# Performance work log

Measured on AMD Instinct MI355X. Metric: run time of the kernel, lower is better.

The kernel has to match this reference:

```python
import jax, jax.numpy as jnp
import numpy as np

LATDIM = 128
ANCHOR_SET_NUM = 64
N_NODES = 10000

def setup_inputs() -> dict:
    key = jax.random.key(0)
    k1, k2, k3, k4, k5 = jax.random.split(key, 5)
    embeds = jax.random.normal(k1, (N_NODES, LATDIM), dtype=jnp.float32)
    dists_array = jax.random.uniform(k2, (ANCHOR_SET_NUM, N_NODES), dtype=jnp.float32)
    W_hidden = jax.random.normal(k3, (LATDIM, 2 * LATDIM), dtype=jnp.float32) * 0.05
    b_hidden = jax.random.normal(k4, (LATDIM,), dtype=jnp.float32) * 0.05
    anchorset_id = jax.random.randint(k5, (ANCHOR_SET_NUM,), 0, N_NODES, dtype=jnp.int64 if jax.config.jax_enable_x64 else jnp.int32)
    return {"embeds": embeds, "dists_array": dists_array, "W_hidden": W_hidden,
            "b_hidden": b_hidden, "anchorset_id": anchorset_id}

def reference(embeds, dists_array, W_hidden, b_hidden, anchorset_id):
    A, N = dists_array.shape
    d = embeds.shape[1]
    set_ids_emb = embeds[anchorset_id]                       # [A, d] anchor gather
    # messages[i, j] = set_ids_emb[j] * dists[j, i]
    messages = set_ids_emb[None, :, :] * dists_array.T[:, :, None]   # [N, A, d]
    # faithful to torch: embeds.repeat(A,1).reshape(-1, A, d) -> embeds[(i*A+j) % N]
    self_feature = jnp.tile(embeds, (A, 1)).reshape(N, A, d)          # [N, A, d]
    m = jnp.concatenate([messages, self_feature], axis=-1)            # [N, A, 2d]
    h = jnp.einsum('nak,ok->nao', m, W_hidden) + b_hidden             # [N, A, d]
    return jnp.mean(h, axis=1)                                        # [N, d]
```

## Files before the change

kernel.cpp:

```cpp
#include <hip/hip_runtime.h>

#define LATDIM 128
#define ANUM   64
#define NNODES 10000
#define PERIOD 625
#define TN     16
#define ABLK   64
#define SBLK   625


__global__ __launch_bounds__(256) void prep_kernel(
    const float* __restrict__ embeds,
    const float* __restrict__ W,
    const float* __restrict__ b,
    const int*   __restrict__ anchor,
    float* __restrict__ P,
    float* __restrict__ T2b)
{
    __shared__ float X_s[LATDIM];
    __shared__ float R_s[LATDIM];
    __shared__ float Xp[8][LATDIM];
    const int tid = threadIdx.x;
    const float4* X_s4 = (const float4*)X_s;

    if (blockIdx.x < ABLK) {
        const int a = blockIdx.x;
        if (tid < 32) {
            ((float4*)X_s)[tid] =
                *((const float4*)(embeds + (size_t)anchor[a] * LATDIM) + tid);
        }
        __syncthreads();

        const int o = tid & 127;
        const int h = tid >> 7;
        const float4* Wr = (const float4*)(W + (size_t)o * (2 * LATDIM) + h * 64);
        float acc = 0.f;
        #pragma unroll
        for (int k4 = 0; k4 < 16; ++k4) {
            float4 w4 = Wr[k4];
            float4 x4 = X_s4[h * 16 + k4];
            acc += w4.x * x4.x + w4.y * x4.y + w4.z * x4.z + w4.w * x4.w;
        }
        if (h == 1) R_s[o] = acc;
        __syncthreads();
        if (h == 0) P[(size_t)a * LATDIM + o] = acc + R_s[o];
    } else {
        const int s = blockIdx.x - ABLK;
        const int row0 = (64 * s) % NNODES;

        const int c4 = tid & 31;
        const int hg = tid >> 5;
        float4 sum = {0.f, 0.f, 0.f, 0.f};
        #pragma unroll
        for (int i = 0; i < 8; ++i) {
            int row = row0 + 8 * i + hg;
            if (row >= NNODES) row -= NNODES;
            float4 v = *((const float4*)(embeds + (size_t)row * LATDIM) + c4);
            sum.x += v.x; sum.y += v.y; sum.z += v.z; sum.w += v.w;
        }
        ((float4*)&Xp[hg][0])[c4] = sum;
        __syncthreads();
        if (tid < LATDIM) {
            float t = Xp[0][tid];
            #pragma unroll
            for (int g = 1; g < 8; ++g) t += Xp[g][tid];
            X_s[tid] = t;
        }
        __syncthreads();

        const int o = tid & 127;
        const int h = tid >> 7;
        const float4* Wr =
            (const float4*)(W + (size_t)o * (2 * LATDIM) + LATDIM + h * 64);
        float acc = 0.f;
        #pragma unroll
        for (int k4 = 0; k4 < 16; ++k4) {
            float4 w4 = Wr[k4];
            float4 x4 = X_s4[h * 16 + k4];
            acc += w4.x * x4.x + w4.y * x4.y + w4.z * x4.z + w4.w * x4.w;
        }
        if (h == 1) R_s[o] = acc;
        __syncthreads();
        if (h == 0)
            T2b[(size_t)s * LATDIM + o] =
                b[o] + (acc + R_s[o]) * (1.0f / ANUM);
    }
}

__global__ __launch_bounds__(256) void main_kernel(
    const float* __restrict__ dists,
    const float* __restrict__ P,
    const float* __restrict__ T2b,
    float* __restrict__ out)
{
    __shared__ float P_s[ANUM * LATDIM];
    const int tid = threadIdx.x;

    {
        float4* P_s4 = (float4*)P_s;
        const float4* Pg = (const float4*)P;
        #pragma unroll
        for (int it = 0; it < (ANUM * LATDIM / 4) / 256; ++it)
            P_s4[it * 256 + tid] = Pg[it * 256 + tid];
    }
    __syncthreads();

    const int lane = tid & 63;
    const int w    = __builtin_amdgcn_readfirstlane(tid >> 6);
    const int o    = (w & 1) * 64 + lane;
    const int nc   = w >> 1;
    const int nb   = blockIdx.x * TN + nc * 8;

    float acc[8] = {};
    #pragma unroll 4
    for (int a = 0; a < ANUM; ++a) {
        const float p = P_s[a * LATDIM + o];
        const float* __restrict__ drow = dists + (size_t)a * NNODES + nb;
        #pragma unroll
        for (int j = 0; j < 8; ++j)
            acc[j] += drow[j] * p;
    }

    #pragma unroll
    for (int j = 0; j < 8; ++j) {
        const int n = nb + j;
        const int s = n % PERIOD;
        out[(size_t)n * LATDIM + o] =
            acc[j] * (1.0f / ANUM) + T2b[(size_t)s * LATDIM + o];
    }
}

extern "C" void kernel_launch(void* const* d_in, const int* in_sizes, int n_in,
                              void* d_out, int out_size, void* d_ws, size_t ws_size,
                              hipStream_t stream) {
    const float* embeds = (const float*)d_in[0];
    const float* dists  = (const float*)d_in[1];
    const float* W      = (const float*)d_in[2];
    const float* b      = (const float*)d_in[3];
    const int*   anchor = (const int*)d_in[4];
    float* out = (float*)d_out;

    float* P   = (float*)d_ws;
    float* T2b = P + ANUM * LATDIM;

    prep_kernel<<<ABLK + SBLK, 256, 0, stream>>>(embeds, W, b, anchor, P, T2b);
    main_kernel<<<NNODES / TN, 256, 0, stream>>>(dists, P, T2b, out);
}
```

Before: 82.37 us.

## Fuse prep and main kernels with a grid-wide atomic barrier

Merges the precompute kernel and the main accumulation kernel into a single launch of 625 blocks. Each block computes one T2b row (plus a P row for the first 64 blocks), then all blocks wait at a software grid barrier built from an atomic counter before reading P. The dists tile is also staged in shared memory with vectorized loads, and the anchor loop is fully unrolled. This removes one kernel launch and the gap between kernels, but adds a memset, relies on all 625 blocks being co-resident, and adds spin-wait time at the barrier.

```diff
diff --git a/kernel.cpp b/kernel.cpp
--- a/kernel.cpp
+++ b/kernel.cpp
@@ -5,49 +5,34 @@
 #define NNODES 10000
 #define PERIOD 625
 #define TN     16
-#define ABLK   64
 #define SBLK   625
 
 
-__global__ __launch_bounds__(256) void prep_kernel(
+__global__ __launch_bounds__(256) void fused_kernel(
     const float* __restrict__ embeds,
+    const float* __restrict__ dists,
     const float* __restrict__ W,
     const float* __restrict__ b,
     const int*   __restrict__ anchor,
     float* __restrict__ P,
-    float* __restrict__ T2b)
+    float* __restrict__ T2b,
+    unsigned int* __restrict__ cnt,
+    float* __restrict__ out)
 {
-    __shared__ float X_s[LATDIM];
-    __shared__ float R_s[LATDIM];
-    __shared__ float Xp[8][LATDIM];
+    __shared__ float P_s[ANUM * LATDIM];
+    __shared__ float D_s[ANUM * TN];
+    float* X_s = P_s;
+    float* R_s = P_s + LATDIM;
+    float (*Xp)[LATDIM] = (float (*)[LATDIM])(P_s + 2 * LATDIM);
+
     const int tid = threadIdx.x;
+    const int bid = blockIdx.x;
+    const int o   = tid & 127;
+    const int h   = tid >> 7;
     const float4* X_s4 = (const float4*)X_s;
 
-    if (blockIdx.x < ABLK) {
-        const int a = blockIdx.x;
-        if (tid < 32) {
-            ((float4*)X_s)[tid] =
-                *((const float4*)(embeds + (size_t)anchor[a] * LATDIM) + tid);
-        }
-        __syncthreads();
-
-        const int o = tid & 127;
-        const int h = tid >> 7;
-        const float4* Wr = (const float4*)(W + (size_t)o * (2 * LATDIM) + h * 64);
-        float acc = 0.f;
-        #pragma unroll
-        for (int k4 = 0; k4 < 16; ++k4) {
-            float4 w4 = Wr[k4];
-            float4 x4 = X_s4[h * 16 + k4];
-            acc += w4.x * x4.x + w4.y * x4.y + w4.z * x4.z + w4.w * x4.w;
-        }
-        if (h == 1) R_s[o] = acc;
-        __syncthreads();
-        if (h == 0) P[(size_t)a * LATDIM + o] = acc + R_s[o];
-    } else {
-        const int s = blockIdx.x - ABLK;
-        const int row0 = (64 * s) % NNODES;
-
+    {
+        const int row0 = (64 * bid) % NNODES;
         const int c4 = tid & 31;
         const int hg = tid >> 5;
         float4 sum = {0.f, 0.f, 0.f, 0.f};
@@ -68,8 +53,6 @@
         }
         __syncthreads();
 
-        const int o = tid & 127;
-        const int h = tid >> 7;
         const float4* Wr =
             (const float4*)(W + (size_t)o * (2 * LATDIM) + LATDIM + h * 64);
         float acc = 0.f;
@@ -82,19 +65,45 @@
         if (h == 1) R_s[o] = acc;
         __syncthreads();
         if (h == 0)
-            T2b[(size_t)s * LATDIM + o] =
+            T2b[(size_t)bid * LATDIM + o] =
                 b[o] + (acc + R_s[o]) * (1.0f / ANUM);
     }
-}
 
-__global__ __launch_bounds__(256) void main_kernel(
-    const float* __restrict__ dists,
-    const float* __restrict__ P,
-    const float* __restrict__ T2b,
-    float* __restrict__ out)
-{
-    __shared__ float P_s[ANUM * LATDIM];
-    const int tid = threadIdx.x;
+    if (bid < ANUM) {
+        __syncthreads();
+        if (tid < 32) {
+            ((float4*)X_s)[tid] =
+                *((const float4*)(embeds + (size_t)anchor[bid] * LATDIM) + tid);
+        }
+        __syncthreads();
+        const float4* Wr = (const float4*)(W + (size_t)o * (2 * LATDIM) + h * 64);
+        float acc = 0.f;
+        #pragma unroll
+        for (int k4 = 0; k4 < 16; ++k4) {
+            float4 w4 = Wr[k4];
+            float4 x4 = X_s4[h * 16 + k4];
+            acc += w4.x * x4.x + w4.y * x4.y + w4.z * x4.z + w4.w * x4.w;
+        }
+        if (h == 1) R_s[o] = acc;
+        __syncthreads();
+        if (h == 0) P[(size_t)bid * LATDIM + o] = acc + R_s[o];
+    }
+
+    __syncthreads();
+    if (tid == 0) {
+        __threadfence();
+        __hip_atomic_fetch_add(cnt, 1u, __ATOMIC_ACQ_REL,
+                               __HIP_MEMORY_SCOPE_AGENT);
+        int guard = 0;
+        while (__hip_atomic_load(cnt, __ATOMIC_ACQUIRE,
+                                 __HIP_MEMORY_SCOPE_AGENT) < (unsigned)SBLK &&
+               guard < (1 << 24)) {
+            __builtin_amdgcn_s_sleep(4);
+            ++guard;
+        }
+    }
+    __syncthreads();
+    __threadfence();
 
     {
         float4* P_s4 = (float4*)P_s;
@@ -102,31 +111,35 @@
         #pragma unroll
         for (int it = 0; it < (ANUM * LATDIM / 4) / 256; ++it)
             P_s4[it * 256 + tid] = Pg[it * 256 + tid];
+        ((float4*)D_s)[tid] = *(const float4*)(
+            dists + (size_t)(tid >> 2) * NNODES + bid * TN + 4 * (tid & 3));
     }
     __syncthreads();
 
     const int lane = tid & 63;
     const int w    = __builtin_amdgcn_readfirstlane(tid >> 6);
-    const int o    = (w & 1) * 64 + lane;
+    const int oo   = (w & 1) * 64 + lane;
     const int nc   = w >> 1;
-    const int nb   = blockIdx.x * TN + nc * 8;
+    const int nb   = bid * TN + nc * 8;
 
     float acc[8] = {};
-    #pragma unroll 4
+    #pragma unroll
     for (int a = 0; a < ANUM; ++a) {
-        const float p = P_s[a * LATDIM + o];
-        const float* __restrict__ drow = dists + (size_t)a * NNODES + nb;
-        #pragma unroll
-        for (int j = 0; j < 8; ++j)
-            acc[j] += drow[j] * p;
+        const float p = P_s[a * LATDIM + oo];
+        const float4 d0 = ((const float4*)(D_s + a * TN + nc * 8))[0];
+        const float4 d1 = ((const float4*)(D_s + a * TN + nc * 8))[1];
+        acc[0] += d0.x * p; acc[1] += d0.y * p;
+        acc[2] += d0.z * p; acc[3] += d0.w * p;
+        acc[4] += d1.x * p; acc[5] += d1.y * p;
+        acc[6] += d1.z * p; acc[7] += d1.w * p;
     }
 
     #pragma unroll
     for (int j = 0; j < 8; ++j) {
         const int n = nb + j;
         const int s = n % PERIOD;
-        out[(size_t)n * LATDIM + o] =
-            acc[j] * (1.0f / ANUM) + T2b[(size_t)s * LATDIM + o];
+        out[(size_t)n * LATDIM + oo] =
+            acc[j] * (1.0f / ANUM) + T2b[(size_t)s * LATDIM + oo];
     }
 }
 
@@ -142,7 +155,9 @@
 
     float* P   = (float*)d_ws;
     float* T2b = P + ANUM * LATDIM;
+    unsigned int* cnt = (unsigned int*)(T2b + PERIOD * LATDIM);
 
-    prep_kernel<<<ABLK + SBLK, 256, 0, stream>>>(embeds, W, b, anchor, P, T2b);
-    main_kernel<<<NNODES / TN, 256, 0, stream>>>(dists, P, T2b, out);
+    hipMemsetAsync(cnt, 0, sizeof(unsigned int), stream);
+    fused_kernel<<<SBLK, 256, 0, stream>>>(embeds, dists, W, b, anchor,
+                                           P, T2b, cnt, out);
 }
```

Measured after the change: 210.2 us. 2.55x slower.

## Fuse prep and main kernels into one per-residue-class kernel

Applied to the files above, without the earlier changes.

Replaces the two-kernel pipeline with a single kernel launched over the 625 residue classes. Each block handles the 16 nodes sharing a self-feature residue. It computes the anchor-weighted dist sums G in shared memory, then applies W to both G and the shared self-feature sum, with a bias-and-mean epilogue. This removes a launch and the workspace round trip. In exchange, every block reloads all 64 anchor embeddings and the full W, the dists reads become strided, and blockIdx is remapped across XCDs.

```diff
diff --git a/kernel.cpp b/kernel.cpp
--- a/kernel.cpp
+++ b/kernel.cpp
@@ -4,52 +4,39 @@
 #define ANUM   64
 #define NNODES 10000
 #define PERIOD 625
-#define TN     16
-#define ABLK   64
-#define SBLK   625
+#define NJ     16
 
 
-__global__ __launch_bounds__(256) void prep_kernel(
+__global__ __launch_bounds__(256) void fused_kernel(
     const float* __restrict__ embeds,
+    const float* __restrict__ dists,
     const float* __restrict__ W,
     const float* __restrict__ b,
     const int*   __restrict__ anchor,
-    float* __restrict__ P,
-    float* __restrict__ T2b)
+    float* __restrict__ out)
 {
-    __shared__ float X_s[LATDIM];
-    __shared__ float R_s[LATDIM];
-    __shared__ float Xp[8][LATDIM];
+    __shared__ float EA[ANUM * LATDIM];
+    __shared__ float G_s[NJ * LATDIM];
+    __shared__ float D_s[ANUM * NJ];
+    __shared__ float S_s[LATDIM];
+    __shared__ int   An[ANUM];
+
     const int tid = threadIdx.x;
-    const float4* X_s4 = (const float4*)X_s;
+    const int orig = blockIdx.x;
+    const int xcd = orig & 7, ii = orig >> 3;
+    const int s = (xcd == 0) ? ii : (79 + (xcd - 1) * 78 + ii);
 
-    if (blockIdx.x < ABLK) {
-        const int a = blockIdx.x;
-        if (tid < 32) {
-            ((float4*)X_s)[tid] =
-                *((const float4*)(embeds + (size_t)anchor[a] * LATDIM) + tid);
-        }
-        __syncthreads();
-
-        const int o = tid & 127;
-        const int h = tid >> 7;
-        const float4* Wr = (const float4*)(W + (size_t)o * (2 * LATDIM) + h * 64);
-        float acc = 0.f;
-        #pragma unroll
-        for (int k4 = 0; k4 < 16; ++k4) {
-            float4 w4 = Wr[k4];
-            float4 x4 = X_s4[h * 16 + k4];
-            acc += w4.x * x4.x + w4.y * x4.y + w4.z * x4.z + w4.w * x4.w;
-        }
-        if (h == 1) R_s[o] = acc;
-        __syncthreads();
-        if (h == 0) P[(size_t)a * LATDIM + o] = acc + R_s[o];
-    } else {
-        const int s = blockIdx.x - ABLK;
+    if (tid < ANUM) An[tid] = anchor[tid];
+    #pragma unroll
+    for (int it = 0; it < 4; ++it) {
+        int idx = it * 256 + tid;
+        int a = idx >> 4, j = idx & 15;
+        D_s[a * NJ + j] = dists[(size_t)a * NNODES + (s + PERIOD * j)];
+    }
+    float (*Xp)[LATDIM] = (float (*)[LATDIM])G_s;
+    {
         const int row0 = (64 * s) % NNODES;
-
-        const int c4 = tid & 31;
-        const int hg = tid >> 5;
+        const int c4 = tid & 31, hg = tid >> 5;
         float4 sum = {0.f, 0.f, 0.f, 0.f};
         #pragma unroll
         for (int i = 0; i < 8; ++i) {
@@ -59,74 +46,81 @@
             sum.x += v.x; sum.y += v.y; sum.z += v.z; sum.w += v.w;
         }
         ((float4*)&Xp[hg][0])[c4] = sum;
-        __syncthreads();
-        if (tid < LATDIM) {
-            float t = Xp[0][tid];
-            #pragma unroll
-            for (int g = 1; g < 8; ++g) t += Xp[g][tid];
-            X_s[tid] = t;
-        }
-        __syncthreads();
-
-        const int o = tid & 127;
-        const int h = tid >> 7;
-        const float4* Wr =
-            (const float4*)(W + (size_t)o * (2 * LATDIM) + LATDIM + h * 64);
-        float acc = 0.f;
-        #pragma unroll
-        for (int k4 = 0; k4 < 16; ++k4) {
-            float4 w4 = Wr[k4];
-            float4 x4 = X_s4[h * 16 + k4];
-            acc += w4.x * x4.x + w4.y * x4.y + w4.z * x4.z + w4.w * x4.w;
-        }
-        if (h == 1) R_s[o] = acc;
-        __syncthreads();
-        if (h == 0)
-            T2b[(size_t)s * LATDIM + o] =
-                b[o] + (acc + R_s[o]) * (1.0f / ANUM);
-    }
-}
-
-__global__ __launch_bounds__(256) void main_kernel(
-    const float* __restrict__ dists,
-    const float* __restrict__ P,
-    const float* __restrict__ T2b,
-    float* __restrict__ out)
-{
-    __shared__ float P_s[ANUM * LATDIM];
-    const int tid = threadIdx.x;
-
-    {
-        float4* P_s4 = (float4*)P_s;
-        const float4* Pg = (const float4*)P;
-        #pragma unroll
-        for (int it = 0; it < (ANUM * LATDIM / 4) / 256; ++it)
-            P_s4[it * 256 + tid] = Pg[it * 256 + tid];
     }
     __syncthreads();
 
-    const int lane = tid & 63;
-    const int w    = __builtin_amdgcn_readfirstlane(tid >> 6);
-    const int o    = (w & 1) * 64 + lane;
-    const int nc   = w >> 1;
-    const int nb   = blockIdx.x * TN + nc * 8;
+    if (tid < LATDIM) {
+        float t = Xp[0][tid];
+        #pragma unroll
+        for (int g = 1; g < 8; ++g) t += Xp[g][tid];
+        S_s[tid] = t;
+    }
+    #pragma unroll
+    for (int it = 0; it < 8; ++it) {
+        int idx = it * 256 + tid;
+        int a = idx >> 5, c4 = idx & 31;
+        ((float4*)EA)[a * 32 + c4] =
+            *((const float4*)(embeds + (size_t)An[a] * LATDIM) + c4);
+    }
+    __syncthreads();
 
-    float acc[8] = {};
-    #pragma unroll 4
-    for (int a = 0; a < ANUM; ++a) {
-        const float p = P_s[a * LATDIM + o];
-        const float* __restrict__ drow = dists + (size_t)a * NNODES + nb;
+    {
+        const int k  = tid & 127;
+        const int jh = tid >> 7;
+        float g[8] = {};
         #pragma unroll
-        for (int j = 0; j < 8; ++j)
-            acc[j] += drow[j] * p;
+        for (int a = 0; a < ANUM; ++a) {
+            const float  ea = EA[a * LATDIM + k];
+            const float4 d0 = ((const float4*)(D_s + a * NJ + jh * 8))[0];
+            const float4 d1 = ((const float4*)(D_s + a * NJ + jh * 8))[1];
+            g[0] += d0.x * ea; g[1] += d0.y * ea;
+            g[2] += d0.z * ea; g[3] += d0.w * ea;
+            g[4] += d1.x * ea; g[5] += d1.y * ea;
+            g[6] += d1.z * ea; g[7] += d1.w * ea;
+        }
+        #pragma unroll
+        for (int jj = 0; jj < 8; ++jj)
+            G_s[(jh * 8 + jj) * LATDIM + k] = g[jj];
     }
+    __syncthreads();
 
-    #pragma unroll
-    for (int j = 0; j < 8; ++j) {
-        const int n = nb + j;
-        const int s = n % PERIOD;
-        out[(size_t)n * LATDIM + o] =
-            acc[j] * (1.0f / ANUM) + T2b[(size_t)s * LATDIM + o];
+    {
+        const int o = tid & 127;
+        const int h = tid >> 7;
+        const float4* Wr1 = (const float4*)(W + (size_t)o * (2 * LATDIM) + h * 64);
+        const float4* Wr2 = (const float4*)(W + (size_t)o * (2 * LATDIM) + LATDIM + h * 64);
+        const float4* S4  = (const float4*)S_s;
+        const float4* G4  = (const float4*)G_s;
+        float acc[NJ] = {};
+        float sacc = 0.f;
+        #pragma unroll
+        for (int q = 0; q < 16; ++q) {
+            const float4 w1 = Wr1[q];
+            const float4 w2 = Wr2[q];
+            const float4 sv = S4[h * 16 + q];
+            sacc += sv.x*w2.x + sv.y*w2.y + sv.z*w2.z + sv.w*w2.w;
+            #pragma unroll
+            for (int j = 0; j < NJ; ++j) {
+                const float4 gv = G4[j * 32 + h * 16 + q];
+                acc[j] += gv.x*w1.x + gv.y*w1.y + gv.z*w1.z + gv.w*w1.w;
+            }
+        }
+        float* R = EA;
+        if (h == 1) {
+            #pragma unroll
+            for (int j = 0; j < NJ; ++j)
+                R[j * LATDIM + o] = acc[j] + sacc;
+        }
+        __syncthreads();
+        if (h == 0) {
+            const float bias = b[o];
+            #pragma unroll
+            for (int j = 0; j < NJ; ++j) {
+                const int n = s + PERIOD * j;
+                out[(size_t)n * LATDIM + o] =
+                    bias + (acc[j] + sacc + R[j * LATDIM + o]) * (1.0f / ANUM);
+            }
+        }
     }
 }
 
@@ -140,9 +134,6 @@
     const int*   anchor = (const int*)d_in[4];
     float* out = (float*)d_out;
 
-    float* P   = (float*)d_ws;
-    float* T2b = P + ANUM * LATDIM;
-
-    prep_kernel<<<ABLK + SBLK, 256, 0, stream>>>(embeds, W, b, anchor, P, T2b);
-    main_kernel<<<NNODES / TN, 256, 0, stream>>>(dists, P, T2b, out);
+    (void)d_ws; (void)ws_size;
+    fused_kernel<<<PERIOD, 256, 0, stream>>>(embeds, dists, W, b, anchor, out);
 }
```

After: 88.13 us. 7.0% more time.

## Fuse periodic self-term computation into main kernel with period-strided node tiling

Applied to the files above, without the earlier changes.

The prep kernel is split: a small kernel computes only the per-anchor projections P. The self-feature projection T2b is now computed inside the main kernel. Each main block handles one period residue s and its 16 nodes n = s + 625*j, so the T2 term is computed once per block and kept in shared memory instead of round-tripping through global memory. Dists columns are staged into shared memory with strided gathers, and blocks are remapped so that XCD-adjacent blocks get contiguous residues. This trades uncoalesced dists loads and strided output rows for removing the T2b intermediate and a larger prep launch.

```diff
diff --git a/kernel.cpp b/kernel.cpp
--- a/kernel.cpp
+++ b/kernel.cpp
@@ -4,52 +4,72 @@
 #define ANUM   64
 #define NNODES 10000
 #define PERIOD 625
-#define TN     16
-#define ABLK   64
-#define SBLK   625
+#define NJ     16
 
 
-__global__ __launch_bounds__(256) void prep_kernel(
+__global__ __launch_bounds__(256) void p_kernel(
     const float* __restrict__ embeds,
     const float* __restrict__ W,
-    const float* __restrict__ b,
     const int*   __restrict__ anchor,
-    float* __restrict__ P,
-    float* __restrict__ T2b)
+    float* __restrict__ P)
 {
     __shared__ float X_s[LATDIM];
     __shared__ float R_s[LATDIM];
+    const int tid = threadIdx.x;
+    const int a = blockIdx.x;
+    if (tid < 32)
+        ((float4*)X_s)[tid] =
+            *((const float4*)(embeds + (size_t)anchor[a] * LATDIM) + tid);
+    __syncthreads();
+    const int o = tid & 127, h = tid >> 7;
+    const float4* Wr = (const float4*)(W + (size_t)o * (2 * LATDIM) + h * 64);
+    const float4* X4 = (const float4*)X_s;
+    float acc = 0.f;
+    #pragma unroll
+    for (int q = 0; q < 16; ++q) {
+        float4 w4 = Wr[q], x4 = X4[h * 16 + q];
+        acc += w4.x*x4.x + w4.y*x4.y + w4.z*x4.z + w4.w*x4.w;
+    }
+    if (h == 1) R_s[o] = acc;
+    __syncthreads();
+    if (h == 0) P[(size_t)a * LATDIM + o] = acc + R_s[o];
+}
+
+__global__ __launch_bounds__(256) void main_kernel(
+    const float* __restrict__ embeds,
+    const float* __restrict__ dists,
+    const float* __restrict__ W,
+    const float* __restrict__ b,
+    const float* __restrict__ P,
+    float* __restrict__ out)
+{
+    __shared__ float P_s[ANUM * LATDIM];
     __shared__ float Xp[8][LATDIM];
+    __shared__ float D_s[ANUM * NJ];
+    __shared__ float S_s[LATDIM];
+    __shared__ float T2_s[LATDIM];
+    __shared__ float Rb[LATDIM];
+
     const int tid = threadIdx.x;
-    const float4* X_s4 = (const float4*)X_s;
+    const int orig = blockIdx.x;
+    const int xcd = orig & 7, ii = orig >> 3;
+    const int s = (xcd == 0) ? ii : (79 + (xcd - 1) * 78 + ii);
 
-    if (blockIdx.x < ABLK) {
-        const int a = blockIdx.x;
-        if (tid < 32) {
-            ((float4*)X_s)[tid] =
-                *((const float4*)(embeds + (size_t)anchor[a] * LATDIM) + tid);
-        }
-        __syncthreads();
-
-        const int o = tid & 127;
-        const int h = tid >> 7;
-        const float4* Wr = (const float4*)(W + (size_t)o * (2 * LATDIM) + h * 64);
-        float acc = 0.f;
+    {
+        float4* P4 = (float4*)P_s; const float4* Pg = (const float4*)P;
         #pragma unroll
-        for (int k4 = 0; k4 < 16; ++k4) {
-            float4 w4 = Wr[k4];
-            float4 x4 = X_s4[h * 16 + k4];
-            acc += w4.x * x4.x + w4.y * x4.y + w4.z * x4.z + w4.w * x4.w;
-        }
-        if (h == 1) R_s[o] = acc;
-        __syncthreads();
-        if (h == 0) P[(size_t)a * LATDIM + o] = acc + R_s[o];
-    } else {
-        const int s = blockIdx.x - ABLK;
+        for (int it = 0; it < 8; ++it)
+            P4[it * 256 + tid] = Pg[it * 256 + tid];
+    }
+    #pragma unroll
+    for (int it = 0; it < 4; ++it) {
+        int idx = it * 256 + tid;
+        int a = idx >> 4, j = idx & 15;
+        D_s[a * NJ + j] = dists[(size_t)a * NNODES + (s + PERIOD * j)];
+    }
+    {
         const int row0 = (64 * s) % NNODES;
-
-        const int c4 = tid & 31;
-        const int hg = tid >> 5;
+        const int c4 = tid & 31, hg = tid >> 5;
         float4 sum = {0.f, 0.f, 0.f, 0.f};
         #pragma unroll
         for (int i = 0; i < 8; ++i) {
@@ -59,49 +79,31 @@
             sum.x += v.x; sum.y += v.y; sum.z += v.z; sum.w += v.w;
         }
         ((float4*)&Xp[hg][0])[c4] = sum;
-        __syncthreads();
-        if (tid < LATDIM) {
-            float t = Xp[0][tid];
-            #pragma unroll
-            for (int g = 1; g < 8; ++g) t += Xp[g][tid];
-            X_s[tid] = t;
-        }
-        __syncthreads();
+    }
+    __syncthreads();
 
-        const int o = tid & 127;
-        const int h = tid >> 7;
-        const float4* Wr =
-            (const float4*)(W + (size_t)o * (2 * LATDIM) + LATDIM + h * 64);
-        float acc = 0.f;
+    if (tid < LATDIM) {
+        float t = Xp[0][tid];
         #pragma unroll
-        for (int k4 = 0; k4 < 16; ++k4) {
-            float4 w4 = Wr[k4];
-            float4 x4 = X_s4[h * 16 + k4];
-            acc += w4.x * x4.x + w4.y * x4.y + w4.z * x4.z + w4.w * x4.w;
-        }
-        if (h == 1) R_s[o] = acc;
-        __syncthreads();
-        if (h == 0)
-            T2b[(size_t)s * LATDIM + o] =
-                b[o] + (acc + R_s[o]) * (1.0f / ANUM);
+        for (int g = 1; g < 8; ++g) t += Xp[g][tid];
+        S_s[tid] = t;
     }
-}
-
-__global__ __launch_bounds__(256) void main_kernel(
-    const float* __restrict__ dists,
-    const float* __restrict__ P,
-    const float* __restrict__ T2b,
-    float* __restrict__ out)
-{
-    __shared__ float P_s[ANUM * LATDIM];
-    const int tid = threadIdx.x;
+    __syncthreads();
 
     {
-        float4* P_s4 = (float4*)P_s;
-        const float4* Pg = (const float4*)P;
+        const int o = tid & 127, h = tid >> 7;
+        const float4* Wr2 =
+            (const float4*)(W + (size_t)o * (2 * LATDIM) + LATDIM + h * 64);
+        const float4* S4 = (const float4*)S_s;
+        float sacc = 0.f;
         #pragma unroll
-        for (int it = 0; it < (ANUM * LATDIM / 4) / 256; ++it)
-            P_s4[it * 256 + tid] = Pg[it * 256 + tid];
+        for (int q = 0; q < 16; ++q) {
+            float4 w4 = Wr2[q], sv = S4[h * 16 + q];
+            sacc += w4.x*sv.x + w4.y*sv.y + w4.z*sv.z + w4.w*sv.w;
+        }
+        if (h == 1) Rb[o] = sacc;
+        __syncthreads();
+        if (h == 0) T2_s[o] = b[o] + (sacc + Rb[o]) * (1.0f / ANUM);
     }
     __syncthreads();
 
@@ -109,24 +111,23 @@
     const int w    = __builtin_amdgcn_readfirstlane(tid >> 6);
     const int o    = (w & 1) * 64 + lane;
     const int nc   = w >> 1;
-    const int nb   = blockIdx.x * TN + nc * 8;
-
     float acc[8] = {};
-    #pragma unroll 4
+    #pragma unroll 8
     for (int a = 0; a < ANUM; ++a) {
         const float p = P_s[a * LATDIM + o];
-        const float* __restrict__ drow = dists + (size_t)a * NNODES + nb;
-        #pragma unroll
-        for (int j = 0; j < 8; ++j)
-            acc[j] += drow[j] * p;
+        const float4 d0 = ((const float4*)(D_s + a * NJ + nc * 8))[0];
+        const float4 d1 = ((const float4*)(D_s + a * NJ + nc * 8))[1];
+        acc[0] += d0.x * p; acc[1] += d0.y * p;
+        acc[2] += d0.z * p; acc[3] += d0.w * p;
+        acc[4] += d1.x * p; acc[5] += d1.y * p;
+        acc[6] += d1.z * p; acc[7] += d1.w * p;
     }
 
+    const float t2 = T2_s[o];
     #pragma unroll
     for (int j = 0; j < 8; ++j) {
-        const int n = nb + j;
-        const int s = n % PERIOD;
-        out[(size_t)n * LATDIM + o] =
-            acc[j] * (1.0f / ANUM) + T2b[(size_t)s * LATDIM + o];
+        const int n = s + PERIOD * (nc * 8 + j);
+        out[(size_t)n * LATDIM + o] = acc[j] * (1.0f / ANUM) + t2;
     }
 }
 
@@ -140,9 +141,8 @@
     const int*   anchor = (const int*)d_in[4];
     float* out = (float*)d_out;
 
-    float* P   = (float*)d_ws;
-    float* T2b = P + ANUM * LATDIM;
+    float* P = (float*)d_ws;
 
-    prep_kernel<<<ABLK + SBLK, 256, 0, stream>>>(embeds, W, b, anchor, P, T2b);
-    main_kernel<<<NNODES / TN, 256, 0, stream>>>(dists, P, T2b, out);
+    p_kernel<<<ANUM, 256, 0, stream>>>(embeds, W, anchor, P);
+    main_kernel<<<PERIOD, 256, 0, stream>>>(embeds, dists, W, b, P, out);
 }
```

New measurement: 84.67 us. 1.03x slower.
